# Performance work log

Measured on AMD Instinct MI355X. Metric: run time of the kernel, lower is better.

The kernel has to match this reference:

```python
import jax, jax.numpy as jnp
import numpy as np

EMBED = 1024
HEADS = 16
HEAD_DIM = EMBED // HEADS
B, S = 4, 1024


def setup_inputs() -> dict:
    key = jax.random.key(0)
    ks = jax.random.split(key, 8)
    return {
        "values": jax.random.normal(ks[0], (B, S, EMBED), dtype=jnp.float32),
        "keys": jax.random.normal(ks[1], (B, S, EMBED), dtype=jnp.float32),
        "query": jax.random.normal(ks[2], (B, S, EMBED), dtype=jnp.float32),
        "mask": jax.random.randint(ks[3], (B, 1, S, S), 0, 2, dtype=jnp.int32),
        "Wv": jax.random.normal(ks[4], (HEAD_DIM, HEAD_DIM), dtype=jnp.float32) / np.sqrt(HEAD_DIM),
        "Wq": jax.random.normal(ks[5], (HEAD_DIM, HEAD_DIM), dtype=jnp.float32) / np.sqrt(HEAD_DIM),
        "Wk": jax.random.normal(ks[6], (HEAD_DIM, HEAD_DIM), dtype=jnp.float32) / np.sqrt(HEAD_DIM),
        "Wu": jax.random.normal(ks[7], (EMBED, EMBED), dtype=jnp.float32) / np.sqrt(EMBED),
        "bu": jnp.zeros((EMBED,), dtype=jnp.float32),
    }


def reference(values, keys, query, mask, Wv, Wq, Wk, Wu, bu):
    n, s, _ = query.shape
    # split heads: [B, S, H, D]
    v = values.reshape(n, s, HEADS, HEAD_DIM)
    k = keys.reshape(n, s, HEADS, HEAD_DIM)
    q = query.reshape(n, s, HEADS, HEAD_DIM)
    # per-head linear (shared weight across heads); torch Linear: x @ W.T
    v = jnp.einsum("nshd,ed->nshe", v, Wv)
    k = jnp.einsum("nshd,ed->nshe", k, Wk)
    q = jnp.einsum("nshd,ed->nshe", q, Wq)
    # scores: [B, H, Q, K]
    dot = jnp.einsum("nqhd,nkhd->nhqk", q, k)
    dot = jnp.where(mask == 0, jnp.float32(-1e20), dot)
    # NOTE: original scales by sqrt(embed_size), not sqrt(head_dim)
    attn = jax.nn.softmax(dot / jnp.sqrt(jnp.float32(EMBED)), axis=3)
    out = jnp.einsum("nhql,nlhd->nqhd", attn, v)
    out = out.reshape(n, s, EMBED)
    return out @ Wu.T + bu
```

## Files before the change

kernel.cpp:

```cpp
#include <hip/hip_runtime.h>
#include <hip/hip_bf16.h>

#define EMBED 1024
#define HEADS 16
#define HDIM  64
#define BATCH 4
#define SEQ   1024

typedef __attribute__((ext_vector_type(8))) short  short8;
typedef __attribute__((ext_vector_type(4))) short  short4v;
typedef __attribute__((ext_vector_type(4))) float  float4v;
typedef __attribute__((ext_vector_type(8))) float  float8;
typedef __attribute__((ext_vector_type(2))) __bf16 bf16x2;
typedef __attribute__((ext_vector_type(8))) __bf16 bf16x8;

static __device__ __forceinline__ short cvt1(float f) {
  return __builtin_bit_cast(short, (__bf16)f);
}

static __device__ __forceinline__ unsigned pkbf(float a, float b) {
  bf16x2 v; v[0] = (__bf16)a; v[1] = (__bf16)b;
  return __builtin_bit_cast(unsigned, v);
}

static __device__ __forceinline__ short8 cvt8(const float* p) {
  float4v a = *(const float4v*)p;
  float4v b = *(const float4v*)(p + 4);
  float8 f = __builtin_shufflevector(a, b, 0, 1, 2, 3, 4, 5, 6, 7);
  bf16x8 bb = __builtin_convertvector(f, bf16x8);
  return __builtin_bit_cast(short8, bb);
}

static __device__ __forceinline__ void block_sync_lds() {
  __builtin_amdgcn_sched_barrier(0);
  asm volatile("s_waitcnt lgkmcnt(0)" ::: "memory");
  __builtin_amdgcn_s_barrier();
  __builtin_amdgcn_sched_barrier(0);
}

#define QSCL 0.04508422002778011f

__global__ __launch_bounds__(256) void k_pre(
    const float* __restrict__ values, const float* __restrict__ keys,
    const float* __restrict__ query,
    const float* __restrict__ Wv, const float* __restrict__ Wq,
    const float* __restrict__ Wk, const float* __restrict__ Wu,
    const int* __restrict__ mask,
    short* __restrict__ qp, short* __restrict__ kp, short* __restrict__ vpT,
    unsigned* __restrict__ mbits, short* __restrict__ wub) {
  const int b = blockIdx.x;
  const int t = threadIdx.x;
  if (b < 1536) {
    const int l = t & 63, lr = l & 15, g = l >> 4;
    const int wbase = (b * 4 + (t >> 6)) * 2;
    const int z = wbase >> 12;
    const float* in_; const float* Wm;
    if (z == 0)      { in_ = query;  Wm = Wq; }
    else if (z == 1) { in_ = keys;   Wm = Wk; }
    else             { in_ = values; Wm = Wv; }
    const float scl = (z == 0) ? QSCL : 1.0f;

    short8 wf0[4], wf1[4];
#pragma unroll
    for (int nt = 0; nt < 4; ++nt) {
      wf0[nt] = cvt8(Wm + (size_t)(nt * 16 + lr) * HDIM + g * 8);
      wf1[nt] = cvt8(Wm + (size_t)(nt * 16 + lr) * HDIM + 32 + g * 8);
    }
    const int rem0 = wbase & 4095,  rem1 = (wbase + 1) & 4095;
    const int h0 = rem0 & 15,       h1 = rem1 & 15;
    const int r00 = (rem0 >> 4) * 16, r01 = (rem1 >> 4) * 16;
    const short8 a00 = cvt8(in_ + (size_t)(r00 + lr) * EMBED + h0 * HDIM + g * 8);
    const short8 a01 = cvt8(in_ + (size_t)(r00 + lr) * EMBED + h0 * HDIM + 32 + g * 8);
    const short8 a10 = cvt8(in_ + (size_t)(r01 + lr) * EMBED + h1 * HDIM + g * 8);
    const short8 a11 = cvt8(in_ + (size_t)(r01 + lr) * EMBED + h1 * HDIM + 32 + g * 8);

    auto unit = [&](short8 aA, short8 aB, int h, int r0) {
      const int n = r0 >> 10, s0 = r0 & 1023;
      const int nh = n * HEADS + h;
      float4v acc[4];
#pragma unroll
      for (int nt = 0; nt < 4; ++nt) {
        acc[nt] = (float4v){0.f, 0.f, 0.f, 0.f};
        acc[nt] = __builtin_amdgcn_mfma_f32_16x16x32_bf16(aA, wf0[nt], acc[nt], 0, 0, 0);
        acc[nt] = __builtin_amdgcn_mfma_f32_16x16x32_bf16(aB, wf1[nt], acc[nt], 0, 0, 0);
      }
      if (z == 2) {
#pragma unroll
        for (int nt = 0; nt < 4; ++nt) {
          short4v r;
          r[0]=cvt1(acc[nt][0]); r[1]=cvt1(acc[nt][1]);
          r[2]=cvt1(acc[nt][2]); r[3]=cvt1(acc[nt][3]);
          *(short4v*)(vpT + (size_t)(nh * HDIM + nt * 16 + lr) * SEQ + s0 + g * 4) = r;
        }
      } else {
        short* outp = (z == 0) ? qp : kp;
        const int b8 = ((s0 >> 4) & 1) * 8;
        const int rbase = s0 & ~31;
#pragma unroll
        for (int nt = 0; nt < 4; ++nt)
#pragma unroll
          for (int i = 0; i < 4; ++i) {
            const int row = (z == 0)
                ? (s0 + g * 4 + i)
                : (rbase + (g & 1) * 16 + b8 + (g >> 1) * 4 + i);
            outp[(size_t)(nh * SEQ + row) * HDIM + nt * 16 + lr] =
                cvt1(acc[nt][i] * scl);
          }
      }
    };
    unit(a00, a01, h0, r00);
    unit(a10, a11, h1, r01);
  } else if (b < 2560) {
    const int tid0 = (b - 1536) * 256 + t;
    const int l = t & 63;
#pragma unroll
    for (int it = 0; it < 16; ++it) {
      int tid = tid0 + it * 262144;
      int v = mask[tid];
      unsigned long long bal = __ballot(v != 0);
      if ((l & 31) == 0) mbits[tid >> 5] = (unsigned)(bal >> (l & 32));
    }
  } else {
    const int base = (b - 2560) * 256 + t;
#pragma unroll
    for (int it = 0; it < 16; ++it) {
      int i4 = (base + it * 16384) * 4;
      float4v v = *(const float4v*)(Wu + i4);
      short4v r; r[0]=cvt1(v[0]); r[1]=cvt1(v[1]); r[2]=cvt1(v[2]); r[3]=cvt1(v[3]);
      *(short4v*)(wub + i4) = r;
    }
  }
}

__global__ __launch_bounds__(256, 4) void k_attn(
    const short* __restrict__ qp, const short* __restrict__ kp,
    const short* __restrict__ vpT, const unsigned* __restrict__ mbits,
    short* __restrict__ ao) {
  const int bid = blockIdx.x;
  const int work = (bid & 7) * 128 + (bid >> 3);
  const int qt = work & 15, grp = work >> 4;
  const int h = grp & 15, n = grp >> 4;

  const int t256 = threadIdx.x;
  const int w = t256 >> 6, l = t256 & 63, lr = l & 15, g = l >> 4;
  const int nh = n * HEADS + h;
  const int q0 = qt * 64 + w * 16;
  const short* qb  = qp  + (size_t)nh * SEQ * HDIM;
  const short* kbp = kp  + (size_t)nh * SEQ * HDIM;
  const short* vb  = vpT + (size_t)nh * HDIM * SEQ;
  const unsigned* mrow = mbits + (size_t)(n * SEQ + q0 + lr) * 32;

  __shared__ __align__(16) short kls0[4096], kls1[4096];
  __shared__ __align__(16) short vls0[4096], vls1[4096];

  const int s0 = t256, s1 = t256 + 256;
  const int r0s = s0 >> 3, c0s = s0 & 7, r1s = s1 >> 3, c1s = s1 & 7;
  const int ld0 = r0s * 64 + ((c0s ^ (r0s & 7)) << 3);
  const int ld1 = r1s * 64 + ((c1s ^ (r1s & 7)) << 3);

  const int e = lr & 7;
  const int base0 = lr * 64 + ((g ^ e) << 3);
  const int base1 = lr * 64 + (((4 + g) ^ e) << 3);

  const short8 qf0 = *(const short8*)(qb + (q0 + lr) * HDIM + g * 8);
  const short8 qf1 = *(const short8*)(qb + (q0 + lr) * HDIM + 32 + g * 8);

  const short8 ones8 = {0x3F80, 0x3F80, 0x3F80, 0x3F80,
                        0x3F80, 0x3F80, 0x3F80, 0x3F80};

  float4v accd[4];
#pragma unroll
  for (int dt = 0; dt < 4; ++dt) accd[dt] = (float4v){0.f, 0.f, 0.f, 0.f};
  float4v lacc = (float4v){0.f, 0.f, 0.f, 0.f};

  auto issue = [&](int tile, short8& K0, short8& K1, short8& V0, short8& V1) {
    const int kn = tile * 64;
    K0 = *(const short8*)(kbp + kn * 64 + s0 * 8);
    K1 = *(const short8*)(kbp + kn * 64 + s1 * 8);
    V0 = *(const short8*)(vb + (size_t)r0s * SEQ + kn + c0s * 8);
    V1 = *(const short8*)(vb + (size_t)r1s * SEQ + kn + c1s * 8);
  };
  auto publish = [&](short* Kd, short* Vd, short8 K0, short8 K1, short8 V0, short8 V1) {
    *(short8*)(Kd + ld0) = K0;
    *(short8*)(Kd + ld1) = K1;
    *(short8*)(Vd + ld0) = V0;
    *(short8*)(Vd + ld1) = V1;
  };
  auto tilec = [&](const short* Kb, const short* Vb, int t) {
    float4v sT[4];
#pragma unroll
    for (int a = 0; a < 4; ++a) {
      short8 kf0 = *(const short8*)(Kb + a * 1024 + base0);
      short8 kf1 = *(const short8*)(Kb + a * 1024 + base1);
      float4v z = (float4v){0.f, 0.f, 0.f, 0.f};
      z = __builtin_amdgcn_mfma_f32_16x16x32_bf16(kf0, qf0, z, 0, 0, 0);
      sT[a] = __builtin_amdgcn_mfma_f32_16x16x32_bf16(kf1, qf1, z, 0, 0, 0);
    }
    uint2 mw = *(const uint2*)(mrow + 2 * t);
    const unsigned t0 = mw.x >> (g * 8);
    const unsigned t1 = mw.y >> (g * 8);
    unsigned dwf[8];
#pragma unroll
    for (int a = 0; a < 4; ++a) {
      unsigned ta = ((a & 2) ? t1 : t0) >> ((a & 1) * 4);
      float p0 = exp2f(sT[a][0]); p0 = (ta & 1u) ? p0 : 0.f;
      float p1 = exp2f(sT[a][1]); p1 = (ta & 2u) ? p1 : 0.f;
      float p2 = exp2f(sT[a][2]); p2 = (ta & 4u) ? p2 : 0.f;
      float p3 = exp2f(sT[a][3]); p3 = (ta & 8u) ? p3 : 0.f;
      dwf[a * 2]     = pkbf(p0, p1);
      dwf[a * 2 + 1] = pkbf(p2, p3);
    }
    short8 pbw0, pbw1;
    __builtin_memcpy(&pbw0, &dwf[0], 16);
    __builtin_memcpy(&pbw1, &dwf[4], 16);
    lacc = __builtin_amdgcn_mfma_f32_16x16x32_bf16(ones8, pbw0, lacc, 0, 0, 0);
    lacc = __builtin_amdgcn_mfma_f32_16x16x32_bf16(ones8, pbw1, lacc, 0, 0, 0);
#pragma unroll
    for (int dt = 0; dt < 4; ++dt) {
      short8 vf0 = *(const short8*)(Vb + dt * 1024 + base0);
      accd[dt] = __builtin_amdgcn_mfma_f32_16x16x32_bf16(vf0, pbw0, accd[dt], 0, 0, 0);
      short8 vf1 = *(const short8*)(Vb + dt * 1024 + base1);
      accd[dt] = __builtin_amdgcn_mfma_f32_16x16x32_bf16(vf1, pbw1, accd[dt], 0, 0, 0);
    }
  };

  short8 aK0, aK1, aV0, aV1;
  short8 bK0, bK1, bV0, bV1;

  issue(0, aK0, aK1, aV0, aV1);
  publish(kls0, vls0, aK0, aK1, aV0, aV1);
  issue(1, bK0, bK1, bV0, bV1);
  block_sync_lds();

  for (int tp = 0; tp < 8; ++tp) {
    if (tp < 7) issue(2 * tp + 2, aK0, aK1, aV0, aV1);
    tilec(kls0, vls0, 2 * tp);
    publish(kls1, vls1, bK0, bK1, bV0, bV1);
    block_sync_lds();
    if (tp < 7) issue(2 * tp + 3, bK0, bK1, bV0, bV1);
    tilec(kls1, vls1, 2 * tp + 1);
    if (tp < 7) {
      publish(kls0, vls0, aK0, aK1, aV0, aV1);
      block_sync_lds();
    }
  }

  float inv = 1.f / fmaxf(lacc[0], 1e-35f);
  short* aorow = ao + (size_t)(n * SEQ + q0 + lr) * EMBED + h * HDIM;
#pragma unroll
  for (int dt = 0; dt < 4; ++dt) {
    short4v r;
    r[0] = cvt1(accd[dt][0] * inv);
    r[1] = cvt1(accd[dt][1] * inv);
    r[2] = cvt1(accd[dt][2] * inv);
    r[3] = cvt1(accd[dt][3] * inv);
    *(short4v*)(aorow + dt * 16 + g * 4) = r;
  }
}

__global__ __launch_bounds__(512, 1) void k_gemm(
    const short* __restrict__ ao, const short* __restrict__ wub,
    const float* __restrict__ bu, float* __restrict__ out) {
  const int r0 = blockIdx.x * 128, c0 = blockIdx.y * 128;
  const int t = threadIdx.x;
  const int w = t >> 6, l = t & 63, lr = l & 15, g = l >> 4;
  const int wr = w >> 2, wc = w & 3;

  __shared__ __align__(16) short als[2][128 * 64];
  __shared__ __align__(16) short bls[2][128 * 64];

  const int ar0 = t >> 3, ac0 = t & 7;
  const int ar1 = (t + 512) >> 3, ac1 = (t + 512) & 7;
  const int ld0 = ar0 * 64 + ((ac0 ^ (ar0 & 7)) << 3);
  const int ld1 = ar1 * 64 + ((ac1 ^ (ar1 & 7)) << 3);
  const short* agp0 = ao  + (size_t)(r0 + ar0) * EMBED + ac0 * 8;
  const short* agp1 = ao  + (size_t)(r0 + ar1) * EMBED + ac1 * 8;
  const short* bgp0 = wub + (size_t)(c0 + ar0) * EMBED + ac0 * 8;
  const short* bgp1 = wub + (size_t)(c0 + ar1) * EMBED + ac1 * 8;

  int aoff[4][2], boff[2][2];
#pragma unroll
  for (int fr = 0; fr < 4; ++fr) {
    const int ra = wr * 64 + fr * 16 + lr;
#pragma unroll
    for (int kk = 0; kk < 2; ++kk)
      aoff[fr][kk] = ra * 64 + (((kk * 4 + g) ^ (ra & 7)) << 3);
  }
#pragma unroll
  for (int fc = 0; fc < 2; ++fc) {
    const int rb = wc * 32 + fc * 16 + lr;
#pragma unroll
    for (int kk = 0; kk < 2; ++kk)
      boff[fc][kk] = rb * 64 + (((kk * 4 + g) ^ (rb & 7)) << 3);
  }

  float4v acc[4][2];
#pragma unroll
  for (int fr = 0; fr < 4; ++fr)
#pragma unroll
    for (int fc = 0; fc < 2; ++fc) acc[fr][fc] = (float4v){0.f, 0.f, 0.f, 0.f};

  {
    short8 a0 = *(const short8*)agp0;
    short8 a1 = *(const short8*)agp1;
    short8 b0 = *(const short8*)bgp0;
    short8 b1 = *(const short8*)bgp1;
    *(short8*)(&als[0][0] + ld0) = a0;
    *(short8*)(&als[0][0] + ld1) = a1;
    *(short8*)(&bls[0][0] + ld0) = b0;
    *(short8*)(&bls[0][0] + ld1) = b1;
  }
  block_sync_lds();

#pragma unroll 2
  for (int tt = 0; tt < 16; ++tt) {
    const int cur = tt & 1, nxt = cur ^ 1;
    short8 sA0, sA1, sB0, sB1;
    if (tt < 15) {
      const int kb = (tt + 1) * 64;
      sA0 = *(const short8*)(agp0 + kb);
      sA1 = *(const short8*)(agp1 + kb);
      sB0 = *(const short8*)(bgp0 + kb);
      sB1 = *(const short8*)(bgp1 + kb);
    }
#pragma unroll
    for (int kk = 0; kk < 2; ++kk) {
      short8 bf0 = *(const short8*)(&bls[cur][0] + boff[0][kk]);
      short8 bf1 = *(const short8*)(&bls[cur][0] + boff[1][kk]);
#pragma unroll
      for (int fr = 0; fr < 4; ++fr) {
        short8 af = *(const short8*)(&als[cur][0] + aoff[fr][kk]);
        acc[fr][0] = __builtin_amdgcn_mfma_f32_16x16x32_bf16(af, bf0, acc[fr][0], 0, 0, 0);
        acc[fr][1] = __builtin_amdgcn_mfma_f32_16x16x32_bf16(af, bf1, acc[fr][1], 0, 0, 0);
      }
    }
    if (tt < 15) {
      *(short8*)(&als[nxt][0] + ld0) = sA0;
      *(short8*)(&als[nxt][0] + ld1) = sA1;
      *(short8*)(&bls[nxt][0] + ld0) = sB0;
      *(short8*)(&bls[nxt][0] + ld1) = sB1;
      block_sync_lds();
    }
  }

#pragma unroll
  for (int fc = 0; fc < 2; ++fc) {
    const int col = c0 + wc * 32 + fc * 16 + lr;
    const float bv = bu[col];
#pragma unroll
    for (int fr = 0; fr < 4; ++fr)
#pragma unroll
      for (int i = 0; i < 4; ++i) {
        const int row = r0 + wr * 64 + fr * 16 + g * 4 + i;
        out[(size_t)row * EMBED + col] = acc[fr][fc][i] + bv;
      }
  }
}

extern "C" void kernel_launch(void* const* d_in, const int* in_sizes, int n_in,
                              void* d_out, int out_size, void* d_ws, size_t ws_size,
                              hipStream_t stream) {
  const float* values = (const float*)d_in[0];
  const float* keys   = (const float*)d_in[1];
  const float* query  = (const float*)d_in[2];
  const int*   mask   = (const int*)d_in[3];
  const float* Wv     = (const float*)d_in[4];
  const float* Wq     = (const float*)d_in[5];
  const float* Wk     = (const float*)d_in[6];
  const float* Wu     = (const float*)d_in[7];
  const float* bu     = (const float*)d_in[8];
  float* out = (float*)d_out;

  char* ws = (char*)d_ws;
  short* qp  = (short*)ws;
  short* kp  = qp + (1u << 22);
  short* vpT = kp + (1u << 22);
  short* ao  = vpT + (1u << 22);
  unsigned* mbits = (unsigned*)(ws + (32u << 20));
  short* wub = (short*)(ws + (32u << 20) + (512u << 10));

  k_pre<<<dim3(2624), 256, 0, stream>>>(values, keys, query, Wv, Wq, Wk, Wu,
                                        mask, qp, kp, vpT, mbits, wub);
  k_attn<<<dim3(1024), 256, 0, stream>>>(qp, kp, vpT, mbits, ao);
  k_gemm<<<dim3(32, 8), 512, 0, stream>>>(ao, wub, bu, out);
}
```

Measured before the change: 82.70 us.

## Process two query tiles per attention block to reuse staged K/V tiles

Each attention workgroup now handles 128 query rows (two 16-row groups per wave) instead of 64, so every K/V tile staged in LDS feeds twice as many MFMAs. The grid is halved to 512 blocks and the launch-bounds occupancy hint drops from 4 to 2 to leave room for the doubled accumulators. exp2f is also replaced with the raw hardware exp2 builtin. The cost is more registers per thread and fewer resident waves, which reduces latency hiding, and 512 blocks may underfill the GPU's 256 CUs at 2 blocks each.

```diff
diff --git a/kernel.cpp b/kernel.cpp
--- a/kernel.cpp
+++ b/kernel.cpp
@@ -21,6 +21,10 @@
 static __device__ __forceinline__ unsigned pkbf(float a, float b) {
   bf16x2 v; v[0] = (__bf16)a; v[1] = (__bf16)b;
   return __builtin_bit_cast(unsigned, v);
+}
+
+static __device__ __forceinline__ float ex2(float x) {
+  return __builtin_amdgcn_exp2f(x);
 }
 
 static __device__ __forceinline__ short8 cvt8(const float* p) {
@@ -132,23 +136,25 @@
   }
 }
 
-__global__ __launch_bounds__(256, 4) void k_attn(
+__global__ __launch_bounds__(256, 2) void k_attn(
     const short* __restrict__ qp, const short* __restrict__ kp,
     const short* __restrict__ vpT, const unsigned* __restrict__ mbits,
     short* __restrict__ ao) {
   const int bid = blockIdx.x;
-  const int work = (bid & 7) * 128 + (bid >> 3);
-  const int qt = work & 15, grp = work >> 4;
+  const int work = (bid & 7) * 64 + (bid >> 3);
+  const int qt = work & 7, grp = work >> 3;
   const int h = grp & 15, n = grp >> 4;
 
   const int t256 = threadIdx.x;
   const int w = t256 >> 6, l = t256 & 63, lr = l & 15, g = l >> 4;
   const int nh = n * HEADS + h;
-  const int q0 = qt * 64 + w * 16;
+  const int q0a = qt * 128 + w * 16;
+  const int q0b = q0a + 64;
   const short* qb  = qp  + (size_t)nh * SEQ * HDIM;
   const short* kbp = kp  + (size_t)nh * SEQ * HDIM;
   const short* vb  = vpT + (size_t)nh * HDIM * SEQ;
-  const unsigned* mrow = mbits + (size_t)(n * SEQ + q0 + lr) * 32;
+  const unsigned* mrowA = mbits + (size_t)(n * SEQ + q0a + lr) * 32;
+  const unsigned* mrowB = mbits + (size_t)(n * SEQ + q0b + lr) * 32;
 
   __shared__ __align__(16) short kls0[4096], kls1[4096];
   __shared__ __align__(16) short vls0[4096], vls1[4096];
@@ -162,16 +168,22 @@
   const int base0 = lr * 64 + ((g ^ e) << 3);
   const int base1 = lr * 64 + (((4 + g) ^ e) << 3);
 
-  const short8 qf0 = *(const short8*)(qb + (q0 + lr) * HDIM + g * 8);
-  const short8 qf1 = *(const short8*)(qb + (q0 + lr) * HDIM + 32 + g * 8);
+  const short8 qa0 = *(const short8*)(qb + (q0a + lr) * HDIM + g * 8);
+  const short8 qa1 = *(const short8*)(qb + (q0a + lr) * HDIM + 32 + g * 8);
+  const short8 qb0 = *(const short8*)(qb + (q0b + lr) * HDIM + g * 8);
+  const short8 qb1 = *(const short8*)(qb + (q0b + lr) * HDIM + 32 + g * 8);
 
   const short8 ones8 = {0x3F80, 0x3F80, 0x3F80, 0x3F80,
                         0x3F80, 0x3F80, 0x3F80, 0x3F80};
 
-  float4v accd[4];
-#pragma unroll
-  for (int dt = 0; dt < 4; ++dt) accd[dt] = (float4v){0.f, 0.f, 0.f, 0.f};
-  float4v lacc = (float4v){0.f, 0.f, 0.f, 0.f};
+  float4v accA[4], accB[4];
+#pragma unroll
+  for (int dt = 0; dt < 4; ++dt) {
+    accA[dt] = (float4v){0.f, 0.f, 0.f, 0.f};
+    accB[dt] = (float4v){0.f, 0.f, 0.f, 0.f};
+  }
+  float4v lacA = (float4v){0.f, 0.f, 0.f, 0.f};
+  float4v lacB = (float4v){0.f, 0.f, 0.f, 0.f};
 
   auto issue = [&](int tile, short8& K0, short8& K1, short8& V0, short8& V1) {
     const int kn = tile * 64;
@@ -187,40 +199,57 @@
     *(short8*)(Vd + ld1) = V1;
   };
   auto tilec = [&](const short* Kb, const short* Vb, int t) {
-    float4v sT[4];
+    float4v sT0[4], sT1[4];
 #pragma unroll
     for (int a = 0; a < 4; ++a) {
       short8 kf0 = *(const short8*)(Kb + a * 1024 + base0);
       short8 kf1 = *(const short8*)(Kb + a * 1024 + base1);
-      float4v z = (float4v){0.f, 0.f, 0.f, 0.f};
-      z = __builtin_amdgcn_mfma_f32_16x16x32_bf16(kf0, qf0, z, 0, 0, 0);
-      sT[a] = __builtin_amdgcn_mfma_f32_16x16x32_bf16(kf1, qf1, z, 0, 0, 0);
-    }
-    uint2 mw = *(const uint2*)(mrow + 2 * t);
-    const unsigned t0 = mw.x >> (g * 8);
-    const unsigned t1 = mw.y >> (g * 8);
-    unsigned dwf[8];
+      float4v z0 = (float4v){0.f, 0.f, 0.f, 0.f};
+      float4v z1 = (float4v){0.f, 0.f, 0.f, 0.f};
+      z0 = __builtin_amdgcn_mfma_f32_16x16x32_bf16(kf0, qa0, z0, 0, 0, 0);
+      sT0[a] = __builtin_amdgcn_mfma_f32_16x16x32_bf16(kf1, qa1, z0, 0, 0, 0);
+      z1 = __builtin_amdgcn_mfma_f32_16x16x32_bf16(kf0, qb0, z1, 0, 0, 0);
+      sT1[a] = __builtin_amdgcn_mfma_f32_16x16x32_bf16(kf1, qb1, z1, 0, 0, 0);
+    }
+    uint2 mwA = *(const uint2*)(mrowA + 2 * t);
+    uint2 mwB = *(const uint2*)(mrowB + 2 * t);
+    const unsigned a0m = mwA.x >> (g * 8), a1m = mwA.y >> (g * 8);
+    const unsigned b0m = mwB.x >> (g * 8), b1m = mwB.y >> (g * 8);
+    unsigned dwA[8], dwB[8];
 #pragma unroll
     for (int a = 0; a < 4; ++a) {
-      unsigned ta = ((a & 2) ? t1 : t0) >> ((a & 1) * 4);
-      float p0 = exp2f(sT[a][0]); p0 = (ta & 1u) ? p0 : 0.f;
-      float p1 = exp2f(sT[a][1]); p1 = (ta & 2u) ? p1 : 0.f;
-      float p2 = exp2f(sT[a][2]); p2 = (ta & 4u) ? p2 : 0.f;
-      float p3 = exp2f(sT[a][3]); p3 = (ta & 8u) ? p3 : 0.f;
-      dwf[a * 2]     = pkbf(p0, p1);
-      dwf[a * 2 + 1] = pkbf(p2, p3);
-    }
-    short8 pbw0, pbw1;
-    __builtin_memcpy(&pbw0, &dwf[0], 16);
-    __builtin_memcpy(&pbw1, &dwf[4], 16);
-    lacc = __builtin_amdgcn_mfma_f32_16x16x32_bf16(ones8, pbw0, lacc, 0, 0, 0);
-    lacc = __builtin_amdgcn_mfma_f32_16x16x32_bf16(ones8, pbw1, lacc, 0, 0, 0);
+      unsigned ta = ((a & 2) ? a1m : a0m) >> ((a & 1) * 4);
+      float p0 = ex2(sT0[a][0]); p0 = (ta & 1u) ? p0 : 0.f;
+      float p1 = ex2(sT0[a][1]); p1 = (ta & 2u) ? p1 : 0.f;
+      float p2 = ex2(sT0[a][2]); p2 = (ta & 4u) ? p2 : 0.f;
+      float p3 = ex2(sT0[a][3]); p3 = (ta & 8u) ? p3 : 0.f;
+      dwA[a * 2]     = pkbf(p0, p1);
+      dwA[a * 2 + 1] = pkbf(p2, p3);
+      unsigned tb = ((a & 2) ? b1m : b0m) >> ((a & 1) * 4);
+      float r0 = ex2(sT1[a][0]); r0 = (tb & 1u) ? r0 : 0.f;
+      float r1 = ex2(sT1[a][1]); r1 = (tb & 2u) ? r1 : 0.f;
+      float r2 = ex2(sT1[a][2]); r2 = (tb & 4u) ? r2 : 0.f;
+      float r3 = ex2(sT1[a][3]); r3 = (tb & 8u) ? r3 : 0.f;
+      dwB[a * 2]     = pkbf(r0, r1);
+      dwB[a * 2 + 1] = pkbf(r2, r3);
+    }
+    short8 pA0, pA1, pB0, pB1;
+    __builtin_memcpy(&pA0, &dwA[0], 16);
+    __builtin_memcpy(&pA1, &dwA[4], 16);
+    __builtin_memcpy(&pB0, &dwB[0], 16);
+    __builtin_memcpy(&pB1, &dwB[4], 16);
+    lacA = __builtin_amdgcn_mfma_f32_16x16x32_bf16(ones8, pA0, lacA, 0, 0, 0);
+    lacA = __builtin_amdgcn_mfma_f32_16x16x32_bf16(ones8, pA1, lacA, 0, 0, 0);
+    lacB = __builtin_amdgcn_mfma_f32_16x16x32_bf16(ones8, pB0, lacB, 0, 0, 0);
+    lacB = __builtin_amdgcn_mfma_f32_16x16x32_bf16(ones8, pB1, lacB, 0, 0, 0);
 #pragma unroll
     for (int dt = 0; dt < 4; ++dt) {
       short8 vf0 = *(const short8*)(Vb + dt * 1024 + base0);
-      accd[dt] = __builtin_amdgcn_mfma_f32_16x16x32_bf16(vf0, pbw0, accd[dt], 0, 0, 0);
+      accA[dt] = __builtin_amdgcn_mfma_f32_16x16x32_bf16(vf0, pA0, accA[dt], 0, 0, 0);
+      accB[dt] = __builtin_amdgcn_mfma_f32_16x16x32_bf16(vf0, pB0, accB[dt], 0, 0, 0);
       short8 vf1 = *(const short8*)(Vb + dt * 1024 + base1);
-      accd[dt] = __builtin_amdgcn_mfma_f32_16x16x32_bf16(vf1, pbw1, accd[dt], 0, 0, 0);
+      accA[dt] = __builtin_amdgcn_mfma_f32_16x16x32_bf16(vf1, pA1, accA[dt], 0, 0, 0);
+      accB[dt] = __builtin_amdgcn_mfma_f32_16x16x32_bf16(vf1, pB1, accB[dt], 0, 0, 0);
     }
   };
 
@@ -245,16 +274,23 @@
     }
   }
 
-  float inv = 1.f / fmaxf(lacc[0], 1e-35f);
-  short* aorow = ao + (size_t)(n * SEQ + q0 + lr) * EMBED + h * HDIM;
+  const float invA = 1.f / fmaxf(lacA[0], 1e-35f);
+  const float invB = 1.f / fmaxf(lacB[0], 1e-35f);
+  short* aorowA = ao + (size_t)(n * SEQ + q0a + lr) * EMBED + h * HDIM;
+  short* aorowB = ao + (size_t)(n * SEQ + q0b + lr) * EMBED + h * HDIM;
 #pragma unroll
   for (int dt = 0; dt < 4; ++dt) {
-    short4v r;
-    r[0] = cvt1(accd[dt][0] * inv);
-    r[1] = cvt1(accd[dt][1] * inv);
-    r[2] = cvt1(accd[dt][2] * inv);
-    r[3] = cvt1(accd[dt][3] * inv);
-    *(short4v*)(aorow + dt * 16 + g * 4) = r;
+    short4v rA, rB;
+    rA[0] = cvt1(accA[dt][0] * invA);
+    rA[1] = cvt1(accA[dt][1] * invA);
+    rA[2] = cvt1(accA[dt][2] * invA);
+    rA[3] = cvt1(accA[dt][3] * invA);
+    rB[0] = cvt1(accB[dt][0] * invB);
+    rB[1] = cvt1(accB[dt][1] * invB);
+    rB[2] = cvt1(accB[dt][2] * invB);
+    rB[3] = cvt1(accB[dt][3] * invB);
+    *(short4v*)(aorowA + dt * 16 + g * 4) = rA;
+    *(short4v*)(aorowB + dt * 16 + g * 4) = rB;
   }
 }
 
@@ -381,6 +417,6 @@
 
   k_pre<<<dim3(2624), 256, 0, stream>>>(values, keys, query, Wv, Wq, Wk, Wu,
                                         mask, qp, kp, vpT, mbits, wub);
-  k_attn<<<dim3(1024), 256, 0, stream>>>(qp, kp, vpT, mbits, ao);
+  k_attn<<<dim3(512), 256, 0, stream>>>(qp, kp, vpT, mbits, ao);
   k_gemm<<<dim3(32, 8), 512, 0, stream>>>(ao, wub, bu, out);
 }
```

Result: faster. 78.25 us (-5.4%).

## Process four query tiles per attention block and pack mask as nibble bytes

Applied to the files above, without the earlier changes.

Each attention block now covers 256 queries (four 64-row subtiles per wave) instead of 64, so every K/V tile staged in LDS feeds four times as many MFMAs. The grid shrinks from 1024 to 256 blocks and launch bounds drop to one block per CU. The mask is repacked as one byte per four keys instead of a bit per key. Separately, the projection kernel handles four units per wave, and exp2 uses the raw hardware builtin. The trade-offs are much higher register pressure, fewer waves to hide latency, and a larger mask buffer to read.

```diff
diff --git a/kernel.cpp b/kernel.cpp
--- a/kernel.cpp
+++ b/kernel.cpp
@@ -21,6 +21,10 @@
 static __device__ __forceinline__ unsigned pkbf(float a, float b) {
   bf16x2 v; v[0] = (__bf16)a; v[1] = (__bf16)b;
   return __builtin_bit_cast(unsigned, v);
+}
+
+static __device__ __forceinline__ float ex2(float x) {
+  return __builtin_amdgcn_exp2f(x);
 }
 
 static __device__ __forceinline__ short8 cvt8(const float* p) {
@@ -47,12 +51,12 @@
     const float* __restrict__ Wk, const float* __restrict__ Wu,
     const int* __restrict__ mask,
     short* __restrict__ qp, short* __restrict__ kp, short* __restrict__ vpT,
-    unsigned* __restrict__ mbits, short* __restrict__ wub) {
+    unsigned char* __restrict__ maskb, short* __restrict__ wub) {
   const int b = blockIdx.x;
   const int t = threadIdx.x;
-  if (b < 1536) {
+  if (b < 768) {
     const int l = t & 63, lr = l & 15, g = l >> 4;
-    const int wbase = (b * 4 + (t >> 6)) * 2;
+    const int wbase = (b * 4 + (t >> 6)) * 4;
     const int z = wbase >> 12;
     const float* in_; const float* Wm;
     if (z == 0)      { in_ = query;  Wm = Wq; }
@@ -60,29 +64,34 @@
     else             { in_ = values; Wm = Wv; }
     const float scl = (z == 0) ? QSCL : 1.0f;
 
+    short8 af0[4], af1[4];
+    int hh[4], rr[4];
+#pragma unroll
+    for (int uu = 0; uu < 4; ++uu) {
+      const int rem = (wbase + uu) & 4095;
+      hh[uu] = rem & 15;
+      rr[uu] = (rem >> 4) * 16;
+      af0[uu] = cvt8(in_ + (size_t)(rr[uu] + lr) * EMBED + hh[uu] * HDIM + g * 8);
+      af1[uu] = cvt8(in_ + (size_t)(rr[uu] + lr) * EMBED + hh[uu] * HDIM + 32 + g * 8);
+    }
     short8 wf0[4], wf1[4];
 #pragma unroll
     for (int nt = 0; nt < 4; ++nt) {
       wf0[nt] = cvt8(Wm + (size_t)(nt * 16 + lr) * HDIM + g * 8);
       wf1[nt] = cvt8(Wm + (size_t)(nt * 16 + lr) * HDIM + 32 + g * 8);
     }
-    const int rem0 = wbase & 4095,  rem1 = (wbase + 1) & 4095;
-    const int h0 = rem0 & 15,       h1 = rem1 & 15;
-    const int r00 = (rem0 >> 4) * 16, r01 = (rem1 >> 4) * 16;
-    const short8 a00 = cvt8(in_ + (size_t)(r00 + lr) * EMBED + h0 * HDIM + g * 8);
-    const short8 a01 = cvt8(in_ + (size_t)(r00 + lr) * EMBED + h0 * HDIM + 32 + g * 8);
-    const short8 a10 = cvt8(in_ + (size_t)(r01 + lr) * EMBED + h1 * HDIM + g * 8);
-    const short8 a11 = cvt8(in_ + (size_t)(r01 + lr) * EMBED + h1 * HDIM + 32 + g * 8);
-
-    auto unit = [&](short8 aA, short8 aB, int h, int r0) {
+
+#pragma unroll
+    for (int uu = 0; uu < 4; ++uu) {
+      const int h = hh[uu], r0 = rr[uu];
       const int n = r0 >> 10, s0 = r0 & 1023;
       const int nh = n * HEADS + h;
       float4v acc[4];
 #pragma unroll
       for (int nt = 0; nt < 4; ++nt) {
         acc[nt] = (float4v){0.f, 0.f, 0.f, 0.f};
-        acc[nt] = __builtin_amdgcn_mfma_f32_16x16x32_bf16(aA, wf0[nt], acc[nt], 0, 0, 0);
-        acc[nt] = __builtin_amdgcn_mfma_f32_16x16x32_bf16(aB, wf1[nt], acc[nt], 0, 0, 0);
+        acc[nt] = __builtin_amdgcn_mfma_f32_16x16x32_bf16(af0[uu], wf0[nt], acc[nt], 0, 0, 0);
+        acc[nt] = __builtin_amdgcn_mfma_f32_16x16x32_bf16(af1[uu], wf1[nt], acc[nt], 0, 0, 0);
       }
       if (z == 2) {
 #pragma unroll
@@ -107,21 +116,19 @@
                 cvt1(acc[nt][i] * scl);
           }
       }
-    };
-    unit(a00, a01, h0, r00);
-    unit(a10, a11, h1, r01);
-  } else if (b < 2560) {
-    const int tid0 = (b - 1536) * 256 + t;
-    const int l = t & 63;
-#pragma unroll
-    for (int it = 0; it < 16; ++it) {
-      int tid = tid0 + it * 262144;
-      int v = mask[tid];
-      unsigned long long bal = __ballot(v != 0);
-      if ((l & 31) == 0) mbits[tid >> 5] = (unsigned)(bal >> (l & 32));
+    }
+  } else if (b < 1280) {
+    const int q0 = ((b - 768) * 8) * 256 + t;
+#pragma unroll
+    for (int it = 0; it < 8; ++it) {
+      const int q = q0 + it * 256;
+      uint4 v = *(const uint4*)(mask + (size_t)q * 4);
+      unsigned nib = (v.x ? 1u : 0u) | (v.y ? 2u : 0u) |
+                     (v.z ? 4u : 0u) | (v.w ? 8u : 0u);
+      maskb[q] = (unsigned char)nib;
     }
   } else {
-    const int base = (b - 2560) * 256 + t;
+    const int base = (b - 1280) * 256 + t;
 #pragma unroll
     for (int it = 0; it < 16; ++it) {
       int i4 = (base + it * 16384) * 4;
@@ -132,23 +139,23 @@
   }
 }
 
-__global__ __launch_bounds__(256, 4) void k_attn(
+__global__ __launch_bounds__(256, 1) void k_attn(
     const short* __restrict__ qp, const short* __restrict__ kp,
-    const short* __restrict__ vpT, const unsigned* __restrict__ mbits,
+    const short* __restrict__ vpT, const unsigned char* __restrict__ maskb,
     short* __restrict__ ao) {
   const int bid = blockIdx.x;
-  const int work = (bid & 7) * 128 + (bid >> 3);
-  const int qt = work & 15, grp = work >> 4;
+  const int work = (bid & 7) * 32 + (bid >> 3);
+  const int qt = work & 3, grp = work >> 2;
   const int h = grp & 15, n = grp >> 4;
 
   const int t256 = threadIdx.x;
   const int w = t256 >> 6, l = t256 & 63, lr = l & 15, g = l >> 4;
   const int nh = n * HEADS + h;
-  const int q0 = qt * 64 + w * 16;
+  const int q00 = qt * 256 + w * 16;
   const short* qb  = qp  + (size_t)nh * SEQ * HDIM;
   const short* kbp = kp  + (size_t)nh * SEQ * HDIM;
   const short* vb  = vpT + (size_t)nh * HDIM * SEQ;
-  const unsigned* mrow = mbits + (size_t)(n * SEQ + q0 + lr) * 32;
+  const unsigned char* mb0 = maskb + (size_t)(n * SEQ + q00 + lr) * 256;
 
   __shared__ __align__(16) short kls0[4096], kls1[4096];
   __shared__ __align__(16) short vls0[4096], vls1[4096];
@@ -162,16 +169,24 @@
   const int base0 = lr * 64 + ((g ^ e) << 3);
   const int base1 = lr * 64 + (((4 + g) ^ e) << 3);
 
-  const short8 qf0 = *(const short8*)(qb + (q0 + lr) * HDIM + g * 8);
-  const short8 qf1 = *(const short8*)(qb + (q0 + lr) * HDIM + 32 + g * 8);
+  short8 qf0[4], qf1[4];
+#pragma unroll
+  for (int x = 0; x < 4; ++x) {
+    qf0[x] = *(const short8*)(qb + (q00 + x * 64 + lr) * HDIM + g * 8);
+    qf1[x] = *(const short8*)(qb + (q00 + x * 64 + lr) * HDIM + 32 + g * 8);
+  }
 
   const short8 ones8 = {0x3F80, 0x3F80, 0x3F80, 0x3F80,
                         0x3F80, 0x3F80, 0x3F80, 0x3F80};
 
-  float4v accd[4];
-#pragma unroll
-  for (int dt = 0; dt < 4; ++dt) accd[dt] = (float4v){0.f, 0.f, 0.f, 0.f};
-  float4v lacc = (float4v){0.f, 0.f, 0.f, 0.f};
+  float4v acc[4][4];
+  float4v lac[4];
+#pragma unroll
+  for (int x = 0; x < 4; ++x) {
+    lac[x] = (float4v){0.f, 0.f, 0.f, 0.f};
+#pragma unroll
+    for (int dt = 0; dt < 4; ++dt) acc[x][dt] = (float4v){0.f, 0.f, 0.f, 0.f};
+  }
 
   auto issue = [&](int tile, short8& K0, short8& K1, short8& V0, short8& V1) {
     const int kn = tile * 64;
@@ -187,40 +202,50 @@
     *(short8*)(Vd + ld1) = V1;
   };
   auto tilec = [&](const short* Kb, const short* Vb, int t) {
-    float4v sT[4];
+    float4v sT[4][4];
 #pragma unroll
     for (int a = 0; a < 4; ++a) {
       short8 kf0 = *(const short8*)(Kb + a * 1024 + base0);
       short8 kf1 = *(const short8*)(Kb + a * 1024 + base1);
-      float4v z = (float4v){0.f, 0.f, 0.f, 0.f};
-      z = __builtin_amdgcn_mfma_f32_16x16x32_bf16(kf0, qf0, z, 0, 0, 0);
-      sT[a] = __builtin_amdgcn_mfma_f32_16x16x32_bf16(kf1, qf1, z, 0, 0, 0);
-    }
-    uint2 mw = *(const uint2*)(mrow + 2 * t);
-    const unsigned t0 = mw.x >> (g * 8);
-    const unsigned t1 = mw.y >> (g * 8);
-    unsigned dwf[8];
-#pragma unroll
-    for (int a = 0; a < 4; ++a) {
-      unsigned ta = ((a & 2) ? t1 : t0) >> ((a & 1) * 4);
-      float p0 = exp2f(sT[a][0]); p0 = (ta & 1u) ? p0 : 0.f;
-      float p1 = exp2f(sT[a][1]); p1 = (ta & 2u) ? p1 : 0.f;
-      float p2 = exp2f(sT[a][2]); p2 = (ta & 4u) ? p2 : 0.f;
-      float p3 = exp2f(sT[a][3]); p3 = (ta & 8u) ? p3 : 0.f;
-      dwf[a * 2]     = pkbf(p0, p1);
-      dwf[a * 2 + 1] = pkbf(p2, p3);
-    }
-    short8 pbw0, pbw1;
-    __builtin_memcpy(&pbw0, &dwf[0], 16);
-    __builtin_memcpy(&pbw1, &dwf[4], 16);
-    lacc = __builtin_amdgcn_mfma_f32_16x16x32_bf16(ones8, pbw0, lacc, 0, 0, 0);
-    lacc = __builtin_amdgcn_mfma_f32_16x16x32_bf16(ones8, pbw1, lacc, 0, 0, 0);
+#pragma unroll
+      for (int x = 0; x < 4; ++x) {
+        float4v z = (float4v){0.f, 0.f, 0.f, 0.f};
+        z = __builtin_amdgcn_mfma_f32_16x16x32_bf16(kf0, qf0[x], z, 0, 0, 0);
+        sT[x][a] = __builtin_amdgcn_mfma_f32_16x16x32_bf16(kf1, qf1[x], z, 0, 0, 0);
+      }
+    }
+    short8 pw0[4], pw1[4];
+#pragma unroll
+    for (int x = 0; x < 4; ++x) {
+      uint4 mv = *(const uint4*)(mb0 + (size_t)x * 64 * 256 + t * 16);
+      const unsigned wl = (g & 2) ? mv.y : mv.x;
+      const unsigned wh = (g & 2) ? mv.w : mv.z;
+      const int sh = (g & 1) * 16;
+      unsigned dw[8];
+#pragma unroll
+      for (int a = 0; a < 4; ++a) {
+        unsigned ta = ((a & 2) ? wh : wl) >> (sh + (a & 1) * 8);
+        float p0 = ex2(sT[x][a][0]); p0 = (ta & 1u) ? p0 : 0.f;
+        float p1 = ex2(sT[x][a][1]); p1 = (ta & 2u) ? p1 : 0.f;
+        float p2 = ex2(sT[x][a][2]); p2 = (ta & 4u) ? p2 : 0.f;
+        float p3 = ex2(sT[x][a][3]); p3 = (ta & 8u) ? p3 : 0.f;
+        dw[a * 2]     = pkbf(p0, p1);
+        dw[a * 2 + 1] = pkbf(p2, p3);
+      }
+      __builtin_memcpy(&pw0[x], &dw[0], 16);
+      __builtin_memcpy(&pw1[x], &dw[4], 16);
+      lac[x] = __builtin_amdgcn_mfma_f32_16x16x32_bf16(ones8, pw0[x], lac[x], 0, 0, 0);
+      lac[x] = __builtin_amdgcn_mfma_f32_16x16x32_bf16(ones8, pw1[x], lac[x], 0, 0, 0);
+    }
 #pragma unroll
     for (int dt = 0; dt < 4; ++dt) {
       short8 vf0 = *(const short8*)(Vb + dt * 1024 + base0);
-      accd[dt] = __builtin_amdgcn_mfma_f32_16x16x32_bf16(vf0, pbw0, accd[dt], 0, 0, 0);
       short8 vf1 = *(const short8*)(Vb + dt * 1024 + base1);
-      accd[dt] = __builtin_amdgcn_mfma_f32_16x16x32_bf16(vf1, pbw1, accd[dt], 0, 0, 0);
+#pragma unroll
+      for (int x = 0; x < 4; ++x) {
+        acc[x][dt] = __builtin_amdgcn_mfma_f32_16x16x32_bf16(vf0, pw0[x], acc[x][dt], 0, 0, 0);
+        acc[x][dt] = __builtin_amdgcn_mfma_f32_16x16x32_bf16(vf1, pw1[x], acc[x][dt], 0, 0, 0);
+      }
     }
   };
 
@@ -245,16 +270,19 @@
     }
   }
 
-  float inv = 1.f / fmaxf(lacc[0], 1e-35f);
-  short* aorow = ao + (size_t)(n * SEQ + q0 + lr) * EMBED + h * HDIM;
-#pragma unroll
-  for (int dt = 0; dt < 4; ++dt) {
-    short4v r;
-    r[0] = cvt1(accd[dt][0] * inv);
-    r[1] = cvt1(accd[dt][1] * inv);
-    r[2] = cvt1(accd[dt][2] * inv);
-    r[3] = cvt1(accd[dt][3] * inv);
-    *(short4v*)(aorow + dt * 16 + g * 4) = r;
+#pragma unroll
+  for (int x = 0; x < 4; ++x) {
+    const float inv = 1.f / fmaxf(lac[x][0], 1e-35f);
+    short* aorow = ao + (size_t)(n * SEQ + q00 + x * 64 + lr) * EMBED + h * HDIM;
+#pragma unroll
+    for (int dt = 0; dt < 4; ++dt) {
+      short4v r;
+      r[0] = cvt1(acc[x][dt][0] * inv);
+      r[1] = cvt1(acc[x][dt][1] * inv);
+      r[2] = cvt1(acc[x][dt][2] * inv);
+      r[3] = cvt1(acc[x][dt][3] * inv);
+      *(short4v*)(aorow + dt * 16 + g * 4) = r;
+    }
   }
 }
 
@@ -376,11 +404,11 @@
   short* kp  = qp + (1u << 22);
   short* vpT = kp + (1u << 22);
   short* ao  = vpT + (1u << 22);
-  unsigned* mbits = (unsigned*)(ws + (32u << 20));
-  short* wub = (short*)(ws + (32u << 20) + (512u << 10));
-
-  k_pre<<<dim3(2624), 256, 0, stream>>>(values, keys, query, Wv, Wq, Wk, Wu,
-                                        mask, qp, kp, vpT, mbits, wub);
-  k_attn<<<dim3(1024), 256, 0, stream>>>(qp, kp, vpT, mbits, ao);
+  unsigned char* maskb = (unsigned char*)(ws + (32u << 20));
+  short* wub = (short*)(ws + (36u << 20));
+
+  k_pre<<<dim3(1344), 256, 0, stream>>>(values, keys, query, Wv, Wq, Wk, Wu,
+                                        mask, qp, kp, vpT, maskb, wub);
+  k_attn<<<dim3(256), 256, 0, stream>>>(qp, kp, vpT, maskb, ao);
   k_gemm<<<dim3(32, 8), 512, 0, stream>>>(ao, wub, bu, out);
 }
```

Measured after the change: 81.31 us. About the same (-1.7%).
